# Performance work log

Measured on AMD Instinct MI355X. Metric: run time of the kernel, lower is better.

The kernel has to match this reference:

```python
import jax, jax.numpy as jnp
import numpy as np

B, S, V, H = 64, 512, 128, 1024
TEMP = 1.0


def _lstm_layer(x_seq, W_ih, W_hh, b_ih, b_hh):
    """x_seq: (S, B, D_in) -> (S, B, H). PyTorch gate order: i, f, g, o."""
    Hh = W_hh.shape[1]
    Bb = x_seq.shape[1]
    # precompute input projections for all timesteps: (S, B, 4H)
    xW = jnp.einsum('sbd,gd->sbg', x_seq, W_ih) + (b_ih + b_hh)

    def step(carry, xw_t):
        h, c = carry
        gates = xw_t + h @ W_hh.T  # (B, 4H)
        i, f, g, o = jnp.split(gates, 4, axis=-1)
        i = jax.nn.sigmoid(i)
        f = jax.nn.sigmoid(f)
        g = jnp.tanh(g)
        o = jax.nn.sigmoid(o)
        c = f * c + i * g
        h = o * jnp.tanh(c)
        return (h, c), h

    h0 = jnp.zeros((Bb, Hh), dtype=x_seq.dtype)
    c0 = jnp.zeros((Bb, Hh), dtype=x_seq.dtype)
    _, hs = jax.lax.scan(step, (h0, c0), xW)
    return hs  # (S, B, H)


def setup_inputs() -> dict:
    key = jax.random.key(0)
    ks = jax.random.split(key, 11)
    s = 1.0 / np.sqrt(H)
    u = lambda k, shape: jax.random.uniform(k, shape, jnp.float32, -s, s)
    return {
        'x': jax.random.normal(ks[0], (B, S, V), jnp.float32),
        'W_ih0': u(ks[1], (4 * H, V)),
        'W_hh0': u(ks[2], (4 * H, H)),
        'b_ih0': u(ks[3], (4 * H,)),
        'b_hh0': u(ks[4], (4 * H,)),
        'W_ih1': u(ks[5], (4 * H, H)),
        'W_hh1': u(ks[6], (4 * H, H)),
        'b_ih1': u(ks[7], (4 * H,)),
        'b_hh1': u(ks[8], (4 * H,)),
        'W_fc': u(ks[9], (V, H)),
        'b_fc': u(ks[10], (V,)),
    }


def reference(x, W_ih0, W_hh0, b_ih0, b_hh0, W_ih1, W_hh1, b_ih1, b_hh1, W_fc, b_fc):
    xs = jnp.transpose(x, (1, 0, 2))  # (S, B, V)
    h1 = _lstm_layer(xs, W_ih0, W_hh0, b_ih0, b_hh0)   # (S, B, H)
    h2 = _lstm_layer(h1, W_ih1, W_hh1, b_ih1, b_hh1)   # (S, B, H)
    logits = jnp.einsum('sbh,vh->sbv', h2, W_fc) + b_fc  # (S, B, V)
    out = jax.nn.log_softmax(logits * TEMP, axis=-1)
    return jnp.transpose(out, (1, 0, 2))  # (B, S, V)
```

## Files before the change

### kernel.cpp

```cpp
#include <hip/hip_runtime.h>
#include <hip/hip_bf16.h>
#include <math.h>


#define S_LEN 512
#define B_SZ  64
#define V_SZ  128
#define H_SZ  1024
#define BH    65536
#define RING  32
#define SLOT  66560
#define FSTR  16
#define INVP  20
#define WSTR  1040

typedef unsigned short u16;
typedef unsigned short u16x8 __attribute__((ext_vector_type(8)));
typedef __bf16         bf16x8 __attribute__((ext_vector_type(8)));
typedef float          f32x4  __attribute__((ext_vector_type(4)));
typedef int            i32x4  __attribute__((ext_vector_type(4)));

__device__ __forceinline__ u16 f2bf(float f) {
    unsigned int u = __float_as_uint(f);
    u += 0x7fffu + ((u >> 16) & 1u);
    return (u16)(u >> 16);
}
__device__ __forceinline__ f32x4 mfma16(u16x8 a, u16x8 b, f32x4 c) {
    return __builtin_amdgcn_mfma_f32_16x16x32_bf16(
        __builtin_bit_cast(bf16x8, a), __builtin_bit_cast(bf16x8, b), c, 0, 0, 0);
}
__device__ __forceinline__ f32x4 mfma16(i32x4 a, u16x8 b, f32x4 c) {
    return __builtin_amdgcn_mfma_f32_16x16x32_bf16(
        __builtin_bit_cast(bf16x8, a), __builtin_bit_cast(bf16x8, b), c, 0, 0, 0);
}

__device__ __forceinline__ void ld_ca(i32x4& d, const u16* p) {
    asm volatile("global_load_dwordx4 %0, %1, off" : "=v"(d) : "v"(p));
}
__device__ __forceinline__ void st_coh16(u16* p, u16x8 v) {
    i32x4 vv = __builtin_bit_cast(i32x4, v);
    asm volatile("global_store_dwordx4 %0, %1, off sc0 sc1" :: "v"(p), "v"(vv));
}
__device__ __forceinline__ int ld_flag(const int* p) {
    int v;
    asm volatile("global_load_dword %0, %1, off sc0 sc1\n\ts_waitcnt vmcnt(0)"
                 : "=v"(v) : "v"(p) : "memory");
    return v;
}
__device__ __forceinline__ void st_flag(int* p, int v) {
    asm volatile("global_store_dword %0, %1, off sc0 sc1" :: "v"(p), "v"(v));
}
__device__ __forceinline__ void poll3(const int* p0, int t0,
                                      const int* p1, int t1,
                                      const int* p2, int t2) {
    for (;;) {
        bool ok = true;
        if (p0) ok = ok && (ld_flag(p0) >= t0);
        if (p1) ok = ok && (ld_flag(p1) >= t1);
        if (p2) ok = ok && (ld_flag(p2) >= t2);
        if (__all(ok)) break;
        __builtin_amdgcn_s_sleep(2);
    }
}
#define WAITV(n) asm volatile("s_waitcnt vmcnt(" #n ")" ::: "memory")
#define LGKM0    asm volatile("s_waitcnt lgkmcnt(0)" ::: "memory")
#define SCHEDB   __builtin_amdgcn_sched_barrier(0)

__device__ __forceinline__ void l2_acquire_inv() {
    __builtin_amdgcn_fence(__ATOMIC_ACQUIRE, "agent");
}

__global__ __launch_bounds__(256) void cvt_kernel(const float* __restrict__ s,
                                                  u16* __restrict__ d, int n)
{
    int i = (blockIdx.x * 256 + threadIdx.x) * 4;
    if (i >= n) return;
    float4 v = *(const float4*)(s + i);
    ushort4 o;
    o.x = f2bf(v.x); o.y = f2bf(v.y); o.z = f2bf(v.z); o.w = f2bf(v.w);
    *(ushort4*)(d + i) = o;
}

union SMemL {
    struct { u16 whh[64 * WSTR]; u16 wih[64 * 144]; u16 tr[4][384]; } l0;
    struct { u16 w[64 * WSTR]; u16 tr[4][384]; } l1;
    float lg[16][132];
};

__global__ __launch_bounds__(256, 1) void persist_kernel(
    const u16* __restrict__ xb,
    const u16* __restrict__ Wih0c, const u16* __restrict__ Whh0c,
    const u16* __restrict__ Wih1c, const u16* __restrict__ Whh1c,
    const u16* __restrict__ Wfcc,
    const float* __restrict__ bih0, const float* __restrict__ bhh0,
    const float* __restrict__ bih1, const float* __restrict__ bhh1,
    const float* __restrict__ bfc,
    u16* __restrict__ h0b, u16* __restrict__ h1b,
    int* __restrict__ flagL0, int* __restrict__ flagL1, int* __restrict__ flagFC,
    float* __restrict__ out)
{
    __shared__ SMemL sm;
    const int bid = blockIdx.x, tid = threadIdx.x;
    const int wave = tid >> 6, lane = tid & 63;
    const int l16 = lane & 15, kgi = lane >> 4, kg8 = kgi * 8;

    if (bid < 64) {
        const int j0 = bid * 16, jj = j0 + l16;
        for (int ch = tid; ch < 1024; ch += 256) {
            int row = ch >> 4, kc = ch & 15;
            int gr = (row >> 4) * H_SZ + j0 + (row & 15);
            *(u16x8*)&sm.l0.wih[row * 144 + kc * 8] =
                *(const u16x8*)(Wih0c + (size_t)gr * V_SZ + kc * 8);
        }
        for (int ch = tid; ch < 8192; ch += 256) {
            int row = ch >> 7, kc = ch & 127;
            int gr = (row >> 4) * H_SZ + j0 + (row & 15);
            *(u16x8*)&sm.l0.whh[row * WSTR + kc * 8] =
                *(const u16x8*)(Whh0c + (size_t)gr * H_SZ + kc * 8);
        }
        __syncthreads();

        const float bii = bih0[jj]            + bhh0[jj];
        const float bif = bih0[H_SZ + jj]     + bhh0[H_SZ + jj];
        const float big = bih0[2 * H_SZ + jj] + bhh0[2 * H_SZ + jj];
        const float bio = bih0[3 * H_SZ + jj] + bhh0[3 * H_SZ + jj];

        int whh_b[4], wih_b[4];
        #pragma unroll
        for (int g = 0; g < 4; ++g) {
            whh_b[g] = (g * 16 + l16) * WSTR + kg8;
            wih_b[g] = (g * 16 + l16) * 144 + kg8;
        }
        const int arow = wave * 16 + l16;
        const u16* xrow = xb + (size_t)arow * (S_LEN * V_SZ);
        u16* trw = sm.l0.tr[wave];
        float creg[4] = {0.f, 0.f, 0.f, 0.f};

        for (int t = 0; t < S_LEN; ++t) {
            f32x4 acc[4][2] = {};
            {
                i32x4 xq[4];
                const u16* xp = xrow + (size_t)t * V_SZ + kg8;
                #pragma unroll
                for (int i = 0; i < 4; ++i) ld_ca(xq[i], xp + i * 32);
                WAITV(0); SCHEDB;
                #pragma unroll
                for (int i = 0; i < 4; ++i)
                    #pragma unroll
                    for (int g = 0; g < 4; ++g)
                        acc[g][i & 1] = mfma16(xq[i],
                            *(const u16x8*)&sm.l0.wih[wih_b[g] + i * 32], acc[g][i & 1]);
            }
            poll3((t >= 1)    ? flagL0 + lane * FSTR        : nullptr, t,
                  (t >= RING) ? flagL1 + lane * FSTR        : nullptr, t - (RING - 1),
                  (t >= RING) ? flagL1 + (64 + lane) * FSTR : nullptr, t - (RING - 1));
            if (t >= INVP && (t % INVP) == 0) l2_acquire_inv();

            auto ISSUE = [&](i32x4 (&buf)[8], const u16* base) {
                #pragma unroll
                for (int q = 0; q < 8; ++q) ld_ca(buf[q], base + q * 32);
            };
            auto COMP = [&](i32x4 (&buf)[8], int k0) {
                #pragma unroll
                for (int q = 0; q < 8; ++q)
                    #pragma unroll
                    for (int g = 0; g < 4; ++g)
                        acc[g][q & 1] = mfma16(buf[q],
                            *(const u16x8*)&sm.l0.whh[whh_b[g] + (k0 + q) * 32],
                            acc[g][q & 1]);
            };
            const u16* aB = h0b + (size_t)((t - 1) & (RING - 1)) * SLOT
                          + (size_t)arow * H_SZ + kg8;
            i32x4 b0[8], b1[8], b2[8];
            ISSUE(b0, aB); ISSUE(b1, aB + 256); ISSUE(b2, aB + 512);
            SCHEDB;
            WAITV(16); SCHEDB; COMP(b0, 0);  ISSUE(b0, aB + 768);
            WAITV(16); SCHEDB; COMP(b1, 8);
            WAITV(8);  SCHEDB; COMP(b2, 16);
            WAITV(0);  SCHEDB; COMP(b0, 24);

            {
                u16* hout = h0b + (size_t)(t & (RING - 1)) * SLOT;
                #pragma unroll
                for (int r = 0; r < 4; ++r) {
                    const float ip = acc[0][0][r] + acc[0][1][r] + bii;
                    const float fp = acc[1][0][r] + acc[1][1][r] + bif;
                    const float gp = acc[2][0][r] + acc[2][1][r] + big;
                    const float op = acc[3][0][r] + acc[3][1][r] + bio;
                    const float iv = 1.f / (1.f + expf(-ip));
                    const float fv = 1.f / (1.f + expf(-fp));
                    const float gv = tanhf(gp);
                    const float ov = 1.f / (1.f + expf(-op));
                    const float cv = fv * creg[r] + iv * gv;
                    creg[r] = cv;
                    trw[(kgi * 4 + r) * 24 + l16] = f2bf(ov * tanhf(cv));
                }
                LGKM0; SCHEDB;
                if (lane < 32) {
                    int m = lane >> 1, jb = lane & 1;
                    u16x8 v = *(const u16x8*)&trw[m * 24 + jb * 8];
                    st_coh16(hout + (size_t)(wave * 16 + m) * H_SZ + j0 + jb * 8, v);
                }
                WAITV(0);
            }
            __syncthreads();
            if (tid == 0) st_flag(flagL0 + bid * FSTR, t + 1);
        }
        return;
    }

    if (bid < 192) {
        const int lb = bid - 64, j0 = lb * 8, jj2 = j0 + (l16 & 7);
        for (int ch = tid; ch < 8192; ch += 256) {
            int ldsrow = ch >> 7, kc = ch & 127;
            int region = ldsrow >> 5, rl = ldsrow & 31;
            int gr = (rl >> 3) * H_SZ + j0 + (rl & 7);
            const u16* src = (region ? Whh1c : Wih1c) + (size_t)gr * H_SZ + kc * 8;
            *(u16x8*)&sm.l1.w[ldsrow * WSTR + kc * 8] = *(const u16x8*)src;
        }
        __syncthreads();

        const float bii = bih1[jj2]            + bhh1[jj2];
        const float bif = bih1[H_SZ + jj2]     + bhh1[H_SZ + jj2];
        const float big = bih1[2 * H_SZ + jj2] + bhh1[2 * H_SZ + jj2];
        const float bio = bih1[3 * H_SZ + jj2] + bhh1[3 * H_SZ + jj2];
        const bool lo = (l16 < 8);

        int wrb[2][2];
        #pragma unroll
        for (int region = 0; region < 2; ++region)
            #pragma unroll
            for (int nt = 0; nt < 2; ++nt)
                wrb[region][nt] = (region * 32 + nt * 16 + l16) * WSTR + kg8;
        const int arow = wave * 16 + l16;
        u16* trw = sm.l1.tr[wave];
        float creg[4] = {0.f, 0.f, 0.f, 0.f};

        for (int t = 0; t < S_LEN; ++t) {
            poll3((t >= 1)    ? flagL1 + lane * FSTR        : nullptr, t,
                  (t >= 1)    ? flagL1 + (64 + lane) * FSTR : nullptr, t,
                  (t >= RING) ? flagFC + (lane & 3) * FSTR  : nullptr, t - (RING - 1));
            if (t >= INVP && (t % INVP) == 0) l2_acquire_inv();

            f32x4 acc[2][2] = {};
            auto ISSUE = [&](i32x4 (&buf)[8], const u16* base) {
                #pragma unroll
                for (int q = 0; q < 8; ++q) ld_ca(buf[q], base + q * 32);
            };
            auto COMP = [&](i32x4 (&buf)[8], int region, int k0) {
                #pragma unroll
                for (int q = 0; q < 8; ++q)
                    #pragma unroll
                    for (int nt = 0; nt < 2; ++nt)
                        acc[nt][q & 1] = mfma16(buf[q],
                            *(const u16x8*)&sm.l1.w[wrb[region][nt] + (k0 + q) * 32],
                            acc[nt][q & 1]);
            };
            const u16* a2 = h1b + (size_t)((t - 1) & (RING - 1)) * SLOT
                          + (size_t)arow * H_SZ + kg8;
            i32x4 b0[8], b1[8], b2[8];
            ISSUE(b0, a2); ISSUE(b1, a2 + 256); ISSUE(b2, a2 + 512);
            SCHEDB;
            WAITV(16); SCHEDB; COMP(b0, 1, 0);  ISSUE(b0, a2 + 768);
            WAITV(16); SCHEDB; COMP(b1, 1, 8);
            WAITV(8);  SCHEDB; COMP(b2, 1, 16);
            WAITV(0);  SCHEDB; COMP(b0, 1, 24);
            poll3(flagL0 + lane * FSTR, t + 1, nullptr, 0, nullptr, 0);
            const u16* a1 = h0b + (size_t)(t & (RING - 1)) * SLOT
                          + (size_t)arow * H_SZ + kg8;
            ISSUE(b0, a1); ISSUE(b1, a1 + 256); ISSUE(b2, a1 + 512);
            SCHEDB;
            WAITV(16); SCHEDB; COMP(b0, 0, 0);  ISSUE(b0, a1 + 768);
            WAITV(16); SCHEDB; COMP(b1, 0, 8);
            WAITV(8);  SCHEDB; COMP(b2, 0, 16);
            WAITV(0);  SCHEDB; COMP(b0, 0, 24);

            {
                #pragma unroll
                for (int r = 0; r < 4; ++r) {
                    const float s0 = acc[0][0][r] + acc[0][1][r];
                    const float s1 = acc[1][0][r] + acc[1][1][r];
                    const float q0 = __shfl_xor(s0, 8);
                    const float q1 = __shfl_xor(s1, 8);
                    const float ip = (lo ? s0 : q0) + bii;
                    const float fp = (lo ? q0 : s0) + bif;
                    const float gp = (lo ? s1 : q1) + big;
                    const float op = (lo ? q1 : s1) + bio;
                    const float iv = 1.f / (1.f + expf(-ip));
                    const float fv = 1.f / (1.f + expf(-fp));
                    const float gv = tanhf(gp);
                    const float ov = 1.f / (1.f + expf(-op));
                    const float cv = fv * creg[r] + iv * gv;
                    creg[r] = cv;
                    if (lo) trw[(kgi * 4 + r) * 24 + (l16 & 7)] = f2bf(ov * tanhf(cv));
                }
                LGKM0; SCHEDB;
                if (lane < 16) {
                    int m = lane;
                    u16x8 v = *(const u16x8*)&trw[m * 24];
                    st_coh16(h1b + (size_t)(t & (RING - 1)) * SLOT
                             + (size_t)(wave * 16 + m) * H_SZ + j0, v);
                }
                WAITV(0);
            }
            __syncthreads();
            if (tid == 0) st_flag(flagL1 + lb * FSTR, t + 1);
        }
        return;
    }

    {
        const int fb = bid - 192, m0 = fb * 16;
        const u16* wp[2];
        #pragma unroll
        for (int nt = 0; nt < 2; ++nt)
            wp[nt] = Wfcc + (size_t)(wave * 32 + nt * 16 + l16) * H_SZ + kg8;

        for (int t = 0; t < S_LEN; ++t) {
            poll3(flagL1 + lane * FSTR, t + 1,
                  flagL1 + (64 + lane) * FSTR, t + 1, nullptr, 0);
            if (t >= INVP && (t % INVP) == 0) l2_acquire_inv();

            const u16* aB = h1b + (size_t)(t & (RING - 1)) * SLOT
                          + (size_t)(m0 + l16) * H_SZ + kg8;
            f32x4 acc[2][2] = {};
            i32x4 buf[8];
            #pragma unroll
            for (int c = 0; c < 4; ++c) {
                #pragma unroll
                for (int q = 0; q < 8; ++q) ld_ca(buf[q], aB + c * 256 + q * 32);
                WAITV(0); SCHEDB;
                #pragma unroll
                for (int q = 0; q < 8; ++q) {
                    #pragma unroll
                    for (int nt = 0; nt < 2; ++nt)
                        acc[nt][q & 1] = mfma16(buf[q],
                            *(const u16x8*)(wp[nt] + (c * 8 + q) * 32), acc[nt][q & 1]);
                }
            }
            #pragma unroll
            for (int nt = 0; nt < 2; ++nt)
                #pragma unroll
                for (int r = 0; r < 4; ++r) {
                    const int m = kgi * 4 + r, n = wave * 32 + nt * 16 + l16;
                    sm.lg[m][n] = acc[nt][0][r] + acc[nt][1][r] + bfc[n];
                }
            __syncthreads();
            const int row = tid >> 4, sub = tid & 15;
            float vals[8]; float mx = -1e30f;
            #pragma unroll
            for (int q = 0; q < 8; ++q) { vals[q] = sm.lg[row][sub * 8 + q]; mx = fmaxf(mx, vals[q]); }
            #pragma unroll
            for (int o = 1; o < 16; o <<= 1) mx = fmaxf(mx, __shfl_xor(mx, o));
            float se = 0.f;
            #pragma unroll
            for (int q = 0; q < 8; ++q) se += expf(vals[q] - mx);
            #pragma unroll
            for (int o = 1; o < 16; o <<= 1) se += __shfl_xor(se, o);
            const float ls = mx + logf(se);
            float* op = out + (size_t)(m0 + row) * (S_LEN * V_SZ) + (size_t)t * V_SZ + sub * 8;
            #pragma unroll
            for (int q = 0; q < 8; ++q) op[q] = vals[q] - ls;

            __syncthreads();
            if (tid == 0) st_flag(flagFC + fb * FSTR, t + 1);
        }
    }
}

extern "C" void kernel_launch(void* const* d_in, const int* in_sizes, int n_in,
                              void* d_out, int out_size, void* d_ws, size_t ws_size,
                              hipStream_t stream)
{
    const float* x    = (const float*)d_in[0];
    const float* Wih0 = (const float*)d_in[1];
    const float* Whh0 = (const float*)d_in[2];
    const float* bih0 = (const float*)d_in[3];
    const float* bhh0 = (const float*)d_in[4];
    const float* Wih1 = (const float*)d_in[5];
    const float* Whh1 = (const float*)d_in[6];
    const float* bih1 = (const float*)d_in[7];
    const float* bhh1 = (const float*)d_in[8];
    const float* Wfc  = (const float*)d_in[9];
    const float* bfc  = (const float*)d_in[10];
    float* out = (float*)d_out;

    u16* wih0 = (u16*)d_ws;
    u16* whh0 = wih0 + (size_t)4096 * 128;
    u16* wih1 = whh0 + (size_t)4096 * 1024;
    u16* whh1 = wih1 + (size_t)4096 * 1024;
    u16* wfc  = whh1 + (size_t)4096 * 1024;
    u16* xbuf = wfc  + (size_t)128 * 1024;
    u16* h0b  = xbuf + (size_t)B_SZ * S_LEN * V_SZ;
    u16* h1b  = h0b + (size_t)RING * SLOT;
    int* flags  = (int*)(h1b + (size_t)RING * SLOT);
    int* flagL0 = flags;
    int* flagL1 = flagL0 + 64 * FSTR;
    int* flagFC = flagL1 + 128 * FSTR;

    auto cvt = [&](const float* s, u16* d, int n) {
        cvt_kernel<<<(n / 4 + 255) / 256, 256, 0, stream>>>(s, d, n);
    };
    cvt(Wih0, wih0, 4096 * 128);
    cvt(Whh0, whh0, 4096 * 1024);
    cvt(Wih1, wih1, 4096 * 1024);
    cvt(Whh1, whh1, 4096 * 1024);
    cvt(Wfc,  wfc,  128 * 1024);
    cvt(x,    xbuf, B_SZ * S_LEN * V_SZ);
    hipMemsetAsync(h0b + (size_t)(RING - 1) * SLOT, 0, (size_t)BH * sizeof(u16), stream);
    hipMemsetAsync(h1b + (size_t)(RING - 1) * SLOT, 0, (size_t)BH * sizeof(u16), stream);
    hipMemsetAsync(flags, 0, (size_t)196 * FSTR * sizeof(int), stream);

    persist_kernel<<<196, 256, 0, stream>>>(
        xbuf, wih0, whh0, wih1, whh1, wfc,
        bih0, bhh0, bih1, bhh1, bfc,
        h0b, h1b, flagL0, flagL1, flagFC, out);
}
```

Before: 6.778 ms.

## Hold LSTM weights in registers and split K across waves with LDS reduction

Result: faster. 6.360 ms (-6.2%).

```diff
diff --git a/kernel.cpp b/kernel.cpp
--- a/kernel.cpp
+++ b/kernel.cpp
@@ -12,7 +12,6 @@
 #define SLOT  66560
 #define FSTR  16
 #define INVP  20
-#define WSTR  1040
 
 typedef unsigned short u16;
 typedef unsigned short u16x8 __attribute__((ext_vector_type(8)));
@@ -70,6 +69,36 @@
     __builtin_amdgcn_fence(__ATOMIC_ACQUIRE, "agent");
 }
 
+#define ISSUE8(buf, base, qp) do {                                          \
+    _Pragma("unroll")                                                       \
+    for (int m_ = 0; m_ < 4; ++m_)                                          \
+        _Pragma("unroll")                                                   \
+        for (int dq_ = 0; dq_ < 2; ++dq_)                                   \
+            ld_ca(buf[m_*2+dq_], (base) + m_*16*H_SZ + (2*(qp)+dq_)*32);    \
+} while (0)
+
+#define COMP_L0(buf, qp) do {                                               \
+    _Pragma("unroll")                                                       \
+    for (int m_ = 0; m_ < 4; ++m_)                                          \
+        _Pragma("unroll")                                                   \
+        for (int dq_ = 0; dq_ < 2; ++dq_)                                   \
+            _Pragma("unroll")                                               \
+            for (int g_ = 0; g_ < 4; ++g_)                                  \
+                acc[m_][g_] = mfma16(buf[m_*2+dq_], Wh[g_][2*(qp)+dq_],     \
+                                     acc[m_][g_]);                          \
+} while (0)
+
+#define COMP_L1(buf, qp) do {                                               \
+    _Pragma("unroll")                                                       \
+    for (int m_ = 0; m_ < 4; ++m_)                                          \
+        _Pragma("unroll")                                                   \
+        for (int dq_ = 0; dq_ < 2; ++dq_)                                   \
+            _Pragma("unroll")                                               \
+            for (int nt_ = 0; nt_ < 2; ++nt_)                               \
+                acc[m_][nt_] = mfma16(buf[m_*2+dq_], Wt[nt_][2*(qp)+dq_],   \
+                                      acc[m_][nt_]);                        \
+} while (0)
+
 __global__ __launch_bounds__(256) void cvt_kernel(const float* __restrict__ s,
                                                   u16* __restrict__ d, int n)
 {
@@ -80,12 +109,6 @@
     o.x = f2bf(v.x); o.y = f2bf(v.y); o.z = f2bf(v.z); o.w = f2bf(v.w);
     *(ushort4*)(d + i) = o;
 }
-
-union SMemL {
-    struct { u16 whh[64 * WSTR]; u16 wih[64 * 144]; u16 tr[4][384]; } l0;
-    struct { u16 w[64 * WSTR]; u16 tr[4][384]; } l1;
-    float lg[16][132];
-};
 
 __global__ __launch_bounds__(256, 1) void persist_kernel(
     const u16* __restrict__ xb,
@@ -99,110 +122,103 @@
     int* __restrict__ flagL0, int* __restrict__ flagL1, int* __restrict__ flagFC,
     float* __restrict__ out)
 {
-    __shared__ SMemL sm;
+    __shared__ union { f32x4 v[4096]; float lg[16][132]; } red;
+    __shared__ u16 trbuf[4][384];
+
     const int bid = blockIdx.x, tid = threadIdx.x;
     const int wave = tid >> 6, lane = tid & 63;
     const int l16 = lane & 15, kgi = lane >> 4, kg8 = kgi * 8;
 
     if (bid < 64) {
         const int j0 = bid * 16, jj = j0 + l16;
-        for (int ch = tid; ch < 1024; ch += 256) {
-            int row = ch >> 4, kc = ch & 15;
-            int gr = (row >> 4) * H_SZ + j0 + (row & 15);
-            *(u16x8*)&sm.l0.wih[row * 144 + kc * 8] =
-                *(const u16x8*)(Wih0c + (size_t)gr * V_SZ + kc * 8);
+        u16x8 Wh[4][8]; u16x8 Wx[4];
+        #pragma unroll
+        for (int g = 0; g < 4; ++g) {
+            const size_t gr = (size_t)(g * H_SZ + jj);
+            #pragma unroll
+            for (int q = 0; q < 8; ++q)
+                Wh[g][q] = *(const u16x8*)(Whh0c + gr * H_SZ + wave * 256 + q * 32 + kg8);
+            Wx[g] = *(const u16x8*)(Wih0c + gr * V_SZ + wave * 32 + kg8);
         }
-        for (int ch = tid; ch < 8192; ch += 256) {
-            int row = ch >> 7, kc = ch & 127;
-            int gr = (row >> 4) * H_SZ + j0 + (row & 15);
-            *(u16x8*)&sm.l0.whh[row * WSTR + kc * 8] =
-                *(const u16x8*)(Whh0c + (size_t)gr * H_SZ + kc * 8);
-        }
-        __syncthreads();
-
         const float bii = bih0[jj]            + bhh0[jj];
         const float bif = bih0[H_SZ + jj]     + bhh0[H_SZ + jj];
         const float big = bih0[2 * H_SZ + jj] + bhh0[2 * H_SZ + jj];
         const float bio = bih0[3 * H_SZ + jj] + bhh0[3 * H_SZ + jj];
 
-        int whh_b[4], wih_b[4];
-        #pragma unroll
-        for (int g = 0; g < 4; ++g) {
-            whh_b[g] = (g * 16 + l16) * WSTR + kg8;
-            wih_b[g] = (g * 16 + l16) * 144 + kg8;
-        }
-        const int arow = wave * 16 + l16;
-        const u16* xrow = xb + (size_t)arow * (S_LEN * V_SZ);
-        u16* trw = sm.l0.tr[wave];
+        const size_t aoff = (size_t)l16 * H_SZ + wave * 256 + kg8;
         float creg[4] = {0.f, 0.f, 0.f, 0.f};
 
         for (int t = 0; t < S_LEN; ++t) {
-            f32x4 acc[4][2] = {};
-            {
-                i32x4 xq[4];
-                const u16* xp = xrow + (size_t)t * V_SZ + kg8;
-                #pragma unroll
-                for (int i = 0; i < 4; ++i) ld_ca(xq[i], xp + i * 32);
-                WAITV(0); SCHEDB;
-                #pragma unroll
-                for (int i = 0; i < 4; ++i)
-                    #pragma unroll
-                    for (int g = 0; g < 4; ++g)
-                        acc[g][i & 1] = mfma16(xq[i],
-                            *(const u16x8*)&sm.l0.wih[wih_b[g] + i * 32], acc[g][i & 1]);
-            }
+            i32x4 xa[4];
+            #pragma unroll
+            for (int m = 0; m < 4; ++m)
+                ld_ca(xa[m], xb + (size_t)(m * 16 + l16) * (S_LEN * V_SZ)
+                              + (size_t)t * V_SZ + wave * 32 + kg8);
             poll3((t >= 1)    ? flagL0 + lane * FSTR        : nullptr, t,
                   (t >= RING) ? flagL1 + lane * FSTR        : nullptr, t - (RING - 1),
                   (t >= RING) ? flagL1 + (64 + lane) * FSTR : nullptr, t - (RING - 1));
             if (t >= INVP && (t % INVP) == 0) l2_acquire_inv();
-
-            auto ISSUE = [&](i32x4 (&buf)[8], const u16* base) {
-                #pragma unroll
-                for (int q = 0; q < 8; ++q) ld_ca(buf[q], base + q * 32);
-            };
-            auto COMP = [&](i32x4 (&buf)[8], int k0) {
-                #pragma unroll
-                for (int q = 0; q < 8; ++q)
-                    #pragma unroll
-                    for (int g = 0; g < 4; ++g)
-                        acc[g][q & 1] = mfma16(buf[q],
-                            *(const u16x8*)&sm.l0.whh[whh_b[g] + (k0 + q) * 32],
-                            acc[g][q & 1]);
-            };
-            const u16* aB = h0b + (size_t)((t - 1) & (RING - 1)) * SLOT
-                          + (size_t)arow * H_SZ + kg8;
-            i32x4 b0[8], b1[8], b2[8];
-            ISSUE(b0, aB); ISSUE(b1, aB + 256); ISSUE(b2, aB + 512);
+            WAITV(0); SCHEDB;
+
+            f32x4 acc[4][4];
+            #pragma unroll
+            for (int m = 0; m < 4; ++m)
+                #pragma unroll
+                for (int g = 0; g < 4; ++g) acc[m][g] = (f32x4){0.f, 0.f, 0.f, 0.f};
+
+            const u16* aB = h0b + (size_t)((t - 1) & (RING - 1)) * SLOT + aoff;
+            i32x4 A0[8], A1[8];
+            ISSUE8(A0, aB, 0); ISSUE8(A1, aB, 1);
             SCHEDB;
-            WAITV(16); SCHEDB; COMP(b0, 0);  ISSUE(b0, aB + 768);
-            WAITV(16); SCHEDB; COMP(b1, 8);
-            WAITV(8);  SCHEDB; COMP(b2, 16);
-            WAITV(0);  SCHEDB; COMP(b0, 24);
-
-            {
-                u16* hout = h0b + (size_t)(t & (RING - 1)) * SLOT;
-                #pragma unroll
-                for (int r = 0; r < 4; ++r) {
-                    const float ip = acc[0][0][r] + acc[0][1][r] + bii;
-                    const float fp = acc[1][0][r] + acc[1][1][r] + bif;
-                    const float gp = acc[2][0][r] + acc[2][1][r] + big;
-                    const float op = acc[3][0][r] + acc[3][1][r] + bio;
-                    const float iv = 1.f / (1.f + expf(-ip));
-                    const float fv = 1.f / (1.f + expf(-fp));
-                    const float gv = tanhf(gp);
-                    const float ov = 1.f / (1.f + expf(-op));
-                    const float cv = fv * creg[r] + iv * gv;
-                    creg[r] = cv;
-                    trw[(kgi * 4 + r) * 24 + l16] = f2bf(ov * tanhf(cv));
+            #pragma unroll
+            for (int m = 0; m < 4; ++m)
+                #pragma unroll
+                for (int g = 0; g < 4; ++g)
+                    acc[m][g] = mfma16(xa[m], Wx[g], acc[m][g]);
+            WAITV(8); SCHEDB; COMP_L0(A0, 0); ISSUE8(A0, aB, 2);
+            WAITV(8); SCHEDB; COMP_L0(A1, 1); ISSUE8(A1, aB, 3);
+            WAITV(8); SCHEDB; COMP_L0(A0, 2);
+            WAITV(0); SCHEDB; COMP_L0(A1, 3);
+
+            #pragma unroll
+            for (int m = 0; m < 4; ++m)
+                #pragma unroll
+                for (int g = 0; g < 4; ++g)
+                    red.v[(wave * 16 + m * 4 + g) * 64 + lane] = acc[m][g];
+            __syncthreads();
+            f32x4 s[4];
+            #pragma unroll
+            for (int g = 0; g < 4; ++g) {
+                s[g] = red.v[(wave * 4 + g) * 64 + lane];
+                #pragma unroll
+                for (int w = 1; w < 4; ++w) {
+                    f32x4 p = red.v[(w * 16 + wave * 4 + g) * 64 + lane];
+                    s[g][0] += p[0]; s[g][1] += p[1]; s[g][2] += p[2]; s[g][3] += p[3];
                 }
-                LGKM0; SCHEDB;
-                if (lane < 32) {
-                    int m = lane >> 1, jb = lane & 1;
-                    u16x8 v = *(const u16x8*)&trw[m * 24 + jb * 8];
-                    st_coh16(hout + (size_t)(wave * 16 + m) * H_SZ + j0 + jb * 8, v);
-                }
-                WAITV(0);
-            }
+            }
+
+            u16* hout = h0b + (size_t)(t & (RING - 1)) * SLOT;
+            #pragma unroll
+            for (int r = 0; r < 4; ++r) {
+                const float ip = s[0][r] + bii;
+                const float fp = s[1][r] + bif;
+                const float gp = s[2][r] + big;
+                const float op = s[3][r] + bio;
+                const float iv = 1.f / (1.f + expf(-ip));
+                const float fv = 1.f / (1.f + expf(-fp));
+                const float gv = tanhf(gp);
+                const float ov = 1.f / (1.f + expf(-op));
+                const float cv = fv * creg[r] + iv * gv;
+                creg[r] = cv;
+                trbuf[wave][(kgi * 4 + r) * 24 + l16] = f2bf(ov * tanhf(cv));
+            }
+            LGKM0; SCHEDB;
+            if (lane < 32) {
+                int m = lane >> 1, jb = lane & 1;
+                u16x8 v = *(const u16x8*)&trbuf[wave][m * 24 + jb * 8];
+                st_coh16(hout + (size_t)(wave * 16 + m) * H_SZ + j0 + jb * 8, v);
+            }
+            WAITV(0);
             __syncthreads();
             if (tid == 0) st_flag(flagL0 + bid * FSTR, t + 1);
         }
@@ -211,98 +227,100 @@
 
     if (bid < 192) {
         const int lb = bid - 64, j0 = lb * 8, jj2 = j0 + (l16 & 7);
-        for (int ch = tid; ch < 8192; ch += 256) {
-            int ldsrow = ch >> 7, kc = ch & 127;
-            int region = ldsrow >> 5, rl = ldsrow & 31;
-            int gr = (rl >> 3) * H_SZ + j0 + (rl & 7);
-            const u16* src = (region ? Whh1c : Wih1c) + (size_t)gr * H_SZ + kc * 8;
-            *(u16x8*)&sm.l1.w[ldsrow * WSTR + kc * 8] = *(const u16x8*)src;
+        const u16* Wsrc = (wave < 2) ? Wih1c : Whh1c;
+        const int kbase = (wave & 1) * 512;
+        u16x8 Wt[2][16];
+        #pragma unroll
+        for (int nt = 0; nt < 2; ++nt) {
+            const int rl = nt * 16 + l16;
+            const size_t gr = (size_t)((rl >> 3) * H_SZ + j0 + (rl & 7));
+            #pragma unroll
+            for (int q = 0; q < 16; ++q)
+                Wt[nt][q] = *(const u16x8*)(Wsrc + gr * H_SZ + kbase + q * 32 + kg8);
         }
-        __syncthreads();
-
         const float bii = bih1[jj2]            + bhh1[jj2];
         const float bif = bih1[H_SZ + jj2]     + bhh1[H_SZ + jj2];
         const float big = bih1[2 * H_SZ + jj2] + bhh1[2 * H_SZ + jj2];
         const float bio = bih1[3 * H_SZ + jj2] + bhh1[3 * H_SZ + jj2];
         const bool lo = (l16 < 8);
 
-        int wrb[2][2];
-        #pragma unroll
-        for (int region = 0; region < 2; ++region)
-            #pragma unroll
-            for (int nt = 0; nt < 2; ++nt)
-                wrb[region][nt] = (region * 32 + nt * 16 + l16) * WSTR + kg8;
-        const int arow = wave * 16 + l16;
-        u16* trw = sm.l1.tr[wave];
+        const size_t aoff = (size_t)l16 * H_SZ + kbase + kg8;
         float creg[4] = {0.f, 0.f, 0.f, 0.f};
 
         for (int t = 0; t < S_LEN; ++t) {
-            poll3((t >= 1)    ? flagL1 + lane * FSTR        : nullptr, t,
-                  (t >= 1)    ? flagL1 + (64 + lane) * FSTR : nullptr, t,
-                  (t >= RING) ? flagFC + (lane & 3) * FSTR  : nullptr, t - (RING - 1));
+            if (wave < 2)
+                poll3(flagL0 + lane * FSTR, t + 1,
+                      (t >= RING) ? flagFC + (lane & 3) * FSTR : nullptr, t - (RING - 1),
+                      nullptr, 0);
+            else
+                poll3((t >= 1)    ? flagL1 + lane * FSTR        : nullptr, t,
+                      (t >= 1)    ? flagL1 + (64 + lane) * FSTR : nullptr, t,
+                      (t >= RING) ? flagFC + (lane & 3) * FSTR  : nullptr, t - (RING - 1));
             if (t >= INVP && (t % INVP) == 0) l2_acquire_inv();
 
-            f32x4 acc[2][2] = {};
-            auto ISSUE = [&](i32x4 (&buf)[8], const u16* base) {
-                #pragma unroll
-                for (int q = 0; q < 8; ++q) ld_ca(buf[q], base + q * 32);
-            };
-            auto COMP = [&](i32x4 (&buf)[8], int region, int k0) {
-                #pragma unroll
-                for (int q = 0; q < 8; ++q)
-                    #pragma unroll
-                    for (int nt = 0; nt < 2; ++nt)
-                        acc[nt][q & 1] = mfma16(buf[q],
-                            *(const u16x8*)&sm.l1.w[wrb[region][nt] + (k0 + q) * 32],
-                            acc[nt][q & 1]);
-            };
-            const u16* a2 = h1b + (size_t)((t - 1) & (RING - 1)) * SLOT
-                          + (size_t)arow * H_SZ + kg8;
-            i32x4 b0[8], b1[8], b2[8];
-            ISSUE(b0, a2); ISSUE(b1, a2 + 256); ISSUE(b2, a2 + 512);
-            SCHEDB;
-            WAITV(16); SCHEDB; COMP(b0, 1, 0);  ISSUE(b0, a2 + 768);
-            WAITV(16); SCHEDB; COMP(b1, 1, 8);
-            WAITV(8);  SCHEDB; COMP(b2, 1, 16);
-            WAITV(0);  SCHEDB; COMP(b0, 1, 24);
-            poll3(flagL0 + lane * FSTR, t + 1, nullptr, 0, nullptr, 0);
-            const u16* a1 = h0b + (size_t)(t & (RING - 1)) * SLOT
-                          + (size_t)arow * H_SZ + kg8;
-            ISSUE(b0, a1); ISSUE(b1, a1 + 256); ISSUE(b2, a1 + 512);
-            SCHEDB;
-            WAITV(16); SCHEDB; COMP(b0, 0, 0);  ISSUE(b0, a1 + 768);
-            WAITV(16); SCHEDB; COMP(b1, 0, 8);
-            WAITV(8);  SCHEDB; COMP(b2, 0, 16);
-            WAITV(0);  SCHEDB; COMP(b0, 0, 24);
-
-            {
-                #pragma unroll
-                for (int r = 0; r < 4; ++r) {
-                    const float s0 = acc[0][0][r] + acc[0][1][r];
-                    const float s1 = acc[1][0][r] + acc[1][1][r];
-                    const float q0 = __shfl_xor(s0, 8);
-                    const float q1 = __shfl_xor(s1, 8);
-                    const float ip = (lo ? s0 : q0) + bii;
-                    const float fp = (lo ? q0 : s0) + bif;
-                    const float gp = (lo ? s1 : q1) + big;
-                    const float op = (lo ? q1 : s1) + bio;
-                    const float iv = 1.f / (1.f + expf(-ip));
-                    const float fv = 1.f / (1.f + expf(-fp));
-                    const float gv = tanhf(gp);
-                    const float ov = 1.f / (1.f + expf(-op));
-                    const float cv = fv * creg[r] + iv * gv;
-                    creg[r] = cv;
-                    if (lo) trw[(kgi * 4 + r) * 24 + (l16 & 7)] = f2bf(ov * tanhf(cv));
+            const u16* aB = ((wave < 2)
+                ? h0b + (size_t)(t & (RING - 1)) * SLOT
+                : h1b + (size_t)((t - 1) & (RING - 1)) * SLOT) + aoff;
+
+            f32x4 acc[4][2];
+            #pragma unroll
+            for (int m = 0; m < 4; ++m)
+                #pragma unroll
+                for (int nt = 0; nt < 2; ++nt) acc[m][nt] = (f32x4){0.f, 0.f, 0.f, 0.f};
+
+            i32x4 A0[8], A1[8];
+            ISSUE8(A0, aB, 0); ISSUE8(A1, aB, 1);
+            WAITV(8); SCHEDB; COMP_L1(A0, 0); ISSUE8(A0, aB, 2);
+            WAITV(8); SCHEDB; COMP_L1(A1, 1); ISSUE8(A1, aB, 3);
+            WAITV(8); SCHEDB; COMP_L1(A0, 2); ISSUE8(A0, aB, 4);
+            WAITV(8); SCHEDB; COMP_L1(A1, 3); ISSUE8(A1, aB, 5);
+            WAITV(8); SCHEDB; COMP_L1(A0, 4); ISSUE8(A0, aB, 6);
+            WAITV(8); SCHEDB; COMP_L1(A1, 5); ISSUE8(A1, aB, 7);
+            WAITV(8); SCHEDB; COMP_L1(A0, 6);
+            WAITV(0); SCHEDB; COMP_L1(A1, 7);
+
+            #pragma unroll
+            for (int m = 0; m < 4; ++m)
+                #pragma unroll
+                for (int nt = 0; nt < 2; ++nt)
+                    red.v[(wave * 16 + m * 2 + nt) * 64 + lane] = acc[m][nt];
+            __syncthreads();
+            f32x4 s[2];
+            #pragma unroll
+            for (int nt = 0; nt < 2; ++nt) {
+                s[nt] = red.v[(wave * 2 + nt) * 64 + lane];
+                #pragma unroll
+                for (int w = 1; w < 4; ++w) {
+                    f32x4 p = red.v[(w * 16 + wave * 2 + nt) * 64 + lane];
+                    s[nt][0] += p[0]; s[nt][1] += p[1]; s[nt][2] += p[2]; s[nt][3] += p[3];
                 }
-                LGKM0; SCHEDB;
-                if (lane < 16) {
-                    int m = lane;
-                    u16x8 v = *(const u16x8*)&trw[m * 24];
-                    st_coh16(h1b + (size_t)(t & (RING - 1)) * SLOT
-                             + (size_t)(wave * 16 + m) * H_SZ + j0, v);
-                }
-                WAITV(0);
-            }
+            }
+
+            #pragma unroll
+            for (int r = 0; r < 4; ++r) {
+                const float s0 = s[0][r];
+                const float s1 = s[1][r];
+                const float q0 = __shfl_xor(s0, 8);
+                const float q1 = __shfl_xor(s1, 8);
+                const float ip = (lo ? s0 : q0) + bii;
+                const float fp = (lo ? q0 : s0) + bif;
+                const float gp = (lo ? s1 : q1) + big;
+                const float op = (lo ? q1 : s1) + bio;
+                const float iv = 1.f / (1.f + expf(-ip));
+                const float fv = 1.f / (1.f + expf(-fp));
+                const float gv = tanhf(gp);
+                const float ov = 1.f / (1.f + expf(-op));
+                const float cv = fv * creg[r] + iv * gv;
+                creg[r] = cv;
+                if (lo) trbuf[wave][(kgi * 4 + r) * 24 + (l16 & 7)] = f2bf(ov * tanhf(cv));
+            }
+            LGKM0; SCHEDB;
+            if (lane < 16) {
+                u16x8 v = *(const u16x8*)&trbuf[wave][lane * 24];
+                st_coh16(h1b + (size_t)(t & (RING - 1)) * SLOT
+                         + (size_t)(wave * 16 + lane) * H_SZ + j0, v);
+            }
+            WAITV(0);
             __syncthreads();
             if (tid == 0) st_flag(flagL1 + lb * FSTR, t + 1);
         }
@@ -343,13 +361,13 @@
                 #pragma unroll
                 for (int r = 0; r < 4; ++r) {
                     const int m = kgi * 4 + r, n = wave * 32 + nt * 16 + l16;
-                    sm.lg[m][n] = acc[nt][0][r] + acc[nt][1][r] + bfc[n];
+                    red.lg[m][n] = acc[nt][0][r] + acc[nt][1][r] + bfc[n];
                 }
             __syncthreads();
             const int row = tid >> 4, sub = tid & 15;
             float vals[8]; float mx = -1e30f;
             #pragma unroll
-            for (int q = 0; q < 8; ++q) { vals[q] = sm.lg[row][sub * 8 + q]; mx = fmaxf(mx, vals[q]); }
+            for (int q = 0; q < 8; ++q) { vals[q] = red.lg[row][sub * 8 + q]; mx = fmaxf(mx, vals[q]); }
             #pragma unroll
             for (int o = 1; o < 16; o <<= 1) mx = fmaxf(mx, __shfl_xor(mx, o));
             float se = 0.f;
```
